# Performance work log

Measured on AMD Instinct MI355X. Metric: run time of the kernel, lower is better.

The kernel has to match this reference:

```python
import jax, jax.numpy as jnp
import numpy as np

N_DT, N_OD = 30000, 10000
D_DT, D_OD = 128, 64
H, O = 128, 64
E1, E2, EL = 500000, 300000, 200000


def _w(k, shape):
    return jax.random.normal(k, shape, jnp.float32) / np.sqrt(shape[0]).astype(np.float32)


def setup_inputs() -> dict:
    key = jax.random.key(0)
    ks = jax.random.split(key, 32)
    inp = {
        "x_dt": jax.random.normal(ks[0], (N_DT, D_DT), jnp.float32),
        "x_od": jax.random.normal(ks[1], (N_OD, D_OD), jnp.float32),
        "ei_dt": jax.random.randint(ks[2], (2, E1), 0, N_DT),
        "ei_rev_src": jax.random.randint(ks[3], (E2,), 0, N_DT),
        "ei_rev_dst": jax.random.randint(ks[4], (E2,), 0, N_OD),
        "el_src": jax.random.randint(ks[5], (EL,), 0, N_OD),
        "el_dst": jax.random.randint(ks[6], (EL,), 0, N_DT),
        # ODEncoderModel params
        "od1_wl": _w(ks[7], (D_DT, H)), "od1_wr": _w(ks[8], (D_DT, H)), "od1_b": jnp.zeros((H,), jnp.float32),
        "od2_wl": _w(ks[9], (H, H)),    "od2_wr": _w(ks[10], (D_OD, H)), "od2_b": jnp.zeros((H,), jnp.float32),
        "od3_wl": _w(ks[11], (H, H)),   "od3_wr": _w(ks[12], (H, H)),    "od3_b": jnp.zeros((H,), jnp.float32),
        "od_lw": _w(ks[13], (H, O)),    "od_lb": jnp.zeros((O,), jnp.float32),
        # DetectorTimeEncoder params
        "dt1_wl": _w(ks[14], (D_DT, H)), "dt1_wr": _w(ks[15], (D_DT, H)), "dt1_b": jnp.zeros((H,), jnp.float32),
        "dt2_wl": _w(ks[16], (H, H)),    "dt2_wr": _w(ks[17], (H, H)),    "dt2_b": jnp.zeros((H,), jnp.float32),
        "dt_lw": _w(ks[18], (H, O)),     "dt_lb": jnp.zeros((O,), jnp.float32),
        # EdgeDecoder params (hidden = out_channels = O)
        "dec_w1": _w(ks[19], (2 * O, O)), "dec_b1": jnp.zeros((O,), jnp.float32),
        "dec_w2": _w(ks[20], (O, 1)),     "dec_b2": jnp.zeros((1,), jnp.float32),
    }
    return inp


def sage(x_src, x_dst, row, col, wl, wr, b, n_dst):
    """PyG SAGEConv (aggr='mean', root_weight=True): lin_l(mean_j x_src[j]) + lin_r(x_dst)."""
    msg = jax.ops.segment_sum(x_src[row], col, num_segments=n_dst)  # [n_dst, d_src]
    cnt = jax.ops.segment_sum(jnp.ones_like(col, dtype=x_src.dtype), col, num_segments=n_dst)
    agg = msg / jnp.maximum(cnt, 1.0)[:, None]
    return agg @ wl + x_dst @ wr + b


def reference(x_dt, x_od, ei_dt, ei_rev_src, ei_rev_dst, el_src, el_dst,
              od1_wl, od1_wr, od1_b, od2_wl, od2_wr, od2_b, od3_wl, od3_wr, od3_b, od_lw, od_lb,
              dt1_wl, dt1_wr, dt1_b, dt2_wl, dt2_wr, dt2_b, dt_lw, dt_lb,
              dec_w1, dec_b1, dec_w2, dec_b2):
    r1, c1 = ei_dt[0], ei_dt[1]
    relu = jax.nn.relu
    # OD encoder: dt metapath conv, then two bipartite convs dt->od
    h = relu(sage(x_dt, x_dt, r1, c1, od1_wl, od1_wr, od1_b, N_DT))
    od = relu(sage(h, x_od, ei_rev_src, ei_rev_dst, od2_wl, od2_wr, od2_b, N_OD))
    od = relu(sage(h, od, ei_rev_src, ei_rev_dst, od3_wl, od3_wr, od3_b, N_OD))
    z_od = od @ od_lw + od_lb  # [N_OD, O]
    # DetectorTime encoder: two homogeneous convs on dt graph
    d = relu(sage(x_dt, x_dt, r1, c1, dt1_wl, dt1_wr, dt1_b, N_DT))
    d = relu(sage(d, d, r1, c1, dt2_wl, dt2_wr, dt2_b, N_DT))
    z_dt = d @ dt_lw + dt_lb  # [N_DT, O]
    # Edge decoder: gather pairs, MLP, sigmoid
    z = jnp.concatenate([z_od[el_src], z_dt[el_dst]], axis=-1)  # [EL, 2O]
    z = relu(z @ dec_w1 + dec_b1)
    return jax.nn.sigmoid(z @ dec_w2 + dec_b2).reshape(-1)  # [EL]
```

## Files before the change

### kernel.cpp

```cpp
#include <hip/hip_runtime.h>
#include <hip/hip_bf16.h>

#define NDT 30000
#define NOD 10000
#define NE1 500000
#define NE2 300000
#define NEL 200000
#define CAP_DT 64
#define CAP_OD 96

typedef unsigned short ushort_t;
typedef unsigned int uint_t;
typedef __attribute__((ext_vector_type(8))) short short8;
typedef __attribute__((ext_vector_type(4))) float f32x4;

static constexpr size_t F_BFUSE = 0;
static constexpr size_t F_ENDF  = 64;
static constexpr size_t U_XDT    = 0;
static constexpr size_t U_XOD    = U_XDT + (size_t)NDT * 128;
static constexpr size_t U_AGGX   = U_XOD + (size_t)NOD * 64;
static constexpr size_t U_H      = U_AGGX + (size_t)NDT * 128;
static constexpr size_t U_D1     = U_H + (size_t)NDT * 128;
static constexpr size_t U_AGGH   = U_D1 + (size_t)NDT * 128;
static constexpr size_t U_OD2    = U_AGGH + (size_t)NOD * 128;
static constexpr size_t U_OD3    = U_OD2 + (size_t)NOD * 128;
static constexpr size_t U_WT1A   = U_OD3 + (size_t)NOD * 128;
static constexpr size_t U_WT1B   = U_WT1A + 32768;
static constexpr size_t U_WTOD2  = U_WT1B + 32768;
static constexpr size_t U_WTOD3  = U_WTOD2 + 24576;
static constexpr size_t U_WTDT2  = U_WTOD3 + 32768;
static constexpr size_t U_WLODT  = U_WTDT2 + 32768;
static constexpr size_t U_WLDTT  = U_WLODT + 8192;
static constexpr size_t U_POD    = U_WLDTT + 8192;
static constexpr size_t U_PDT    = U_POD + (size_t)NOD * 64;
static constexpr size_t U_SRC_DT = U_PDT + (size_t)NDT * 64;
static constexpr size_t U_SRC_OD = U_SRC_DT + (size_t)NDT * CAP_DT;
static constexpr size_t U_END    = U_SRC_OD + (size_t)NOD * CAP_OD;
static constexpr size_t I_CNT_DT = 0;
static constexpr size_t I_CNT_OD = 30000;

__device__ __forceinline__ ushort_t f2bf(float f) {
    uint_t u = __float_as_uint(f);
    return (ushort_t)((u + 0x7fffu + ((u >> 16) & 1u)) >> 16);
}
__device__ __forceinline__ float bf2f(uint_t lo16) { return __uint_as_float(lo16 << 16); }

static constexpr int NB_FILL = (NE1 / 4 + 255) / 256;
static constexpr int NB_CONV = ((NDT * 128 + NOD * 64) / 4 + 255) / 256;
static constexpr int NB_WT   = (155648 + 255) / 256;
static constexpr int NB_FUSE = (16448 + 255) / 256;
static constexpr int NB_PF   = NB_FILL + NB_CONV + NB_WT + NB_FUSE;

struct PFArgs {
    const int *r1, *c1, *rev_src, *rev_dst;
    int *cnt_dt, *cnt_od;
    ushort_t *srcs_dt, *srcs_od;
    const float *x_dt, *x_od;
    ushort_t *xdt_bf, *xod_bf;
    const float *od1_wl, *od1_wr, *dt1_wl, *dt1_wr;
    const float *od2_wl, *od2_wr, *od3_wl, *od3_wr, *dt2_wl, *dt2_wr;
    ushort_t *wt1a, *wt1b, *wtod2, *wtod3, *wtdt2;
    const float *od_lw, *od_lb, *dt_lw, *dt_lb, *w1, *b1;
    ushort_t *wodt, *wdtt;
    float *bfuse;
};

__global__ __launch_bounds__(256) void prep_fill(PFArgs p) {
    int blk = blockIdx.x;
    int tid = threadIdx.x;
    if (blk < NB_FILL) {
        int b = (blk * 256 + tid) * 4;
        if (b + 3 < NE1) {
            int4 d = *(const int4*)(p.c1 + b);
            int4 s = *(const int4*)(p.r1 + b);
            int p0 = atomicAdd(&p.cnt_dt[d.x], 1);
            int p1 = atomicAdd(&p.cnt_dt[d.y], 1);
            int p2 = atomicAdd(&p.cnt_dt[d.z], 1);
            int p3 = atomicAdd(&p.cnt_dt[d.w], 1);
            if (p0 < CAP_DT) p.srcs_dt[d.x * CAP_DT + p0] = (ushort_t)s.x;
            if (p1 < CAP_DT) p.srcs_dt[d.y * CAP_DT + p1] = (ushort_t)s.y;
            if (p2 < CAP_DT) p.srcs_dt[d.z * CAP_DT + p2] = (ushort_t)s.z;
            if (p3 < CAP_DT) p.srcs_dt[d.w * CAP_DT + p3] = (ushort_t)s.w;
        } else {
            for (int i = b; i < NE1; i++) {
                int q = atomicAdd(&p.cnt_dt[p.c1[i]], 1);
                if (q < CAP_DT) p.srcs_dt[p.c1[i] * CAP_DT + q] = (ushort_t)p.r1[i];
            }
        }
        if (b + 3 < NE2) {
            int4 d = *(const int4*)(p.rev_dst + b);
            int4 s = *(const int4*)(p.rev_src + b);
            int p0 = atomicAdd(&p.cnt_od[d.x], 1);
            int p1 = atomicAdd(&p.cnt_od[d.y], 1);
            int p2 = atomicAdd(&p.cnt_od[d.z], 1);
            int p3 = atomicAdd(&p.cnt_od[d.w], 1);
            if (p0 < CAP_OD) p.srcs_od[d.x * CAP_OD + p0] = (ushort_t)s.x;
            if (p1 < CAP_OD) p.srcs_od[d.y * CAP_OD + p1] = (ushort_t)s.y;
            if (p2 < CAP_OD) p.srcs_od[d.z * CAP_OD + p2] = (ushort_t)s.z;
            if (p3 < CAP_OD) p.srcs_od[d.w * CAP_OD + p3] = (ushort_t)s.w;
        } else if (b < NE2) {
            for (int i = b; i < NE2; i++) {
                int q = atomicAdd(&p.cnt_od[p.rev_dst[i]], 1);
                if (q < CAP_OD) p.srcs_od[p.rev_dst[i] * CAP_OD + q] = (ushort_t)p.rev_src[i];
            }
        }
        return;
    }
    blk -= NB_FILL;
    if (blk < NB_CONV) {
        size_t i4 = ((size_t)blk * 256 + tid) * 4;
        const size_t n_dt = (size_t)NDT * 128, n_od = (size_t)NOD * 64;
        if (i4 < n_dt) {
            float4 v = *(const float4*)(p.x_dt + i4);
            ushort4 o = { f2bf(v.x), f2bf(v.y), f2bf(v.z), f2bf(v.w) };
            *(ushort4*)(p.xdt_bf + i4) = o;
        } else if (i4 - n_dt < n_od) {
            size_t j = i4 - n_dt;
            float4 v = *(const float4*)(p.x_od + j);
            ushort4 o = { f2bf(v.x), f2bf(v.y), f2bf(v.z), f2bf(v.w) };
            *(ushort4*)(p.xod_bf + j) = o;
        }
        return;
    }
    blk -= NB_CONV;
    if (blk < NB_WT) {
        int i = blk * 256 + tid;
        const float* wl; const float* wr; ushort_t* dst; int q, KT;
        if (i < 32768)       { q = i;          KT = 256; wl = p.od1_wl; wr = p.od1_wr; dst = p.wt1a; }
        else if (i < 65536)  { q = i - 32768;  KT = 256; wl = p.dt1_wl; wr = p.dt1_wr; dst = p.wt1b; }
        else if (i < 90112)  { q = i - 65536;  KT = 192; wl = p.od2_wl; wr = p.od2_wr; dst = p.wtod2; }
        else if (i < 122880) { q = i - 90112;  KT = 256; wl = p.od3_wl; wr = p.od3_wr; dst = p.wtod3; }
        else if (i < 155648) { q = i - 122880; KT = 256; wl = p.dt2_wl; wr = p.dt2_wr; dst = p.wtdt2; }
        else return;
        int n = q / KT, k = q - n * KT;
        float v = (k < 128) ? wl[(size_t)k * 128 + n] : wr[(size_t)(k - 128) * 128 + n];
        dst[q] = f2bf(v);
        return;
    }
    blk -= NB_WT;
    {
        int i = blk * 256 + tid;
        if (i < 8192) {
            int r = i >> 6, q = i & 63;
            float s = 0.f;
            for (int j = 0; j < 64; j++) s = fmaf(p.od_lw[r * 64 + j], p.w1[j * 64 + q], s);
            p.wodt[q * 128 + r] = f2bf(s);
        } else if (i < 16384) {
            int w = i - 8192, r = w >> 6, q = w & 63;
            float s = 0.f;
            for (int j = 0; j < 64; j++) s = fmaf(p.dt_lw[r * 64 + j], p.w1[(64 + j) * 64 + q], s);
            p.wdtt[q * 128 + r] = f2bf(s);
        } else if (i < 16448) {
            int q = i - 16384;
            float s = p.b1[q];
            for (int j = 0; j < 64; j++) {
                s = fmaf(p.od_lb[j], p.w1[j * 64 + q], s);
                s = fmaf(p.dt_lb[j], p.w1[(64 + j) * 64 + q], s);
            }
            p.bfuse[q] = s;
        }
    }
}

__device__ __forceinline__ void seg_mean_body(const ushort_t* __restrict__ X,
                                              const int* __restrict__ cnt,
                                              const ushort_t* __restrict__ srcs, int cap,
                                              ushort_t* __restrict__ out, int b, int t) {
    int deg = cnt[b];
    int n = deg < cap ? deg : cap;
    int start = b * cap;
    float lo[8] = {}, hi[8] = {};
    int j = 0;
    for (; j + 7 < n; j += 8) {
        uint_t v[8];
#pragma unroll
        for (int u = 0; u < 8; u++) {
            int s = srcs[start + j + u];
            v[u] = *(const uint_t*)&X[(size_t)s * 128 + 2 * t];
        }
#pragma unroll
        for (int u = 0; u < 8; u++) {
            lo[u] += bf2f(v[u] & 0xffff);
            hi[u] += __uint_as_float(v[u] & 0xffff0000u);
        }
    }
    for (; j < n; j++) {
        uint_t v = *(const uint_t*)&X[(size_t)srcs[start + j] * 128 + 2 * t];
        lo[0] += bf2f(v & 0xffff);
        hi[0] += __uint_as_float(v & 0xffff0000u);
    }
    float inv = deg > 0 ? 1.f / (float)deg : 0.f;
    float s0 = (((lo[0] + lo[1]) + (lo[2] + lo[3])) + ((lo[4] + lo[5]) + (lo[6] + lo[7]))) * inv;
    float s1 = (((hi[0] + hi[1]) + (hi[2] + hi[3])) + ((hi[4] + hi[5]) + (hi[6] + hi[7]))) * inv;
    *(uint_t*)&out[(size_t)b * 128 + 2 * t] = (uint_t)f2bf(s0) | ((uint_t)f2bf(s1) << 16);
}

__global__ __launch_bounds__(64) void seg_mean_bf(const ushort_t* __restrict__ X,
                                                  const int* __restrict__ cnt,
                                                  const ushort_t* __restrict__ srcs, int cap,
                                                  ushort_t* __restrict__ out) {
    seg_mean_body(X, cnt, srcs, cap, out, blockIdx.x, threadIdx.x);
}

__global__ __launch_bounds__(64) void seg_mean2(const ushort_t* Xa, const int* cnta, const ushort_t* srca,
                                                int capa, ushort_t* outa, int Na,
                                                const ushort_t* Xb, const int* cntb, const ushort_t* srcb,
                                                int capb, ushort_t* outb) {
    int b = blockIdx.x;
    if (b < Na) seg_mean_body(Xa, cnta, srca, capa, outa, b, threadIdx.x);
    else        seg_mean_body(Xb, cntb, srcb, capb, outb, b - Na, threadIdx.x);
}

template <bool DUAL>
__global__ __launch_bounds__(256) void sage_mfma(
    const ushort_t* __restrict__ A1, int K1,
    const ushort_t* __restrict__ A2, int K2,
    const ushort_t* __restrict__ Wta, const ushort_t* __restrict__ Wtb,
    const float* __restrict__ ba, const float* __restrict__ bb,
    ushort_t* __restrict__ outa, ushort_t* __restrict__ outb, int M) {
    __shared__ __align__(16) ushort_t As[32 * 264];
    __shared__ __align__(16) ushort_t Wsa[128 * 40];
    __shared__ __align__(16) ushort_t Wsb[DUAL ? 128 * 40 : 8];
    const int KT = K1 + K2;
    const int AST = KT + 8;
    int t = threadIdx.x;
    int lane = t & 63, wave = t >> 6;
    int quad = lane >> 4, l16 = lane & 15;
    int mtile = wave & 1, nquad = wave >> 1;
    int mb = blockIdx.x * 32;

    int c1n = 32 * (K1 >> 3);
    for (int c = t; c < c1n; c += 256) {
        int row = c / (K1 >> 3), k8 = (c % (K1 >> 3)) * 8;
        int m = mb + row; if (m >= M) m = M - 1;
        *(short8*)&As[row * AST + k8] = *(const short8*)&A1[(size_t)m * K1 + k8];
    }
    int c2n = 32 * (K2 >> 3);
    for (int c = t; c < c2n; c += 256) {
        int row = c / (K2 >> 3), k8 = (c % (K2 >> 3)) * 8;
        int m = mb + row; if (m >= M) m = M - 1;
        *(short8*)&As[row * AST + K1 + k8] = *(const short8*)&A2[(size_t)m * K2 + k8];
    }
    f32x4 acca[4] = {};
    f32x4 accb[4] = {};
    for (int kc = 0; kc < KT; kc += 32) {
        __syncthreads();
        for (int c = t; c < 512; c += 256) {
            int n = c >> 2, k8 = (c & 3) * 8;
            *(short8*)&Wsa[n * 40 + k8] = *(const short8*)&Wta[(size_t)n * KT + kc + k8];
            if (DUAL)
                *(short8*)&Wsb[n * 40 + k8] = *(const short8*)&Wtb[(size_t)n * KT + kc + k8];
        }
        __syncthreads();
        short8 af = *(const short8*)&As[(mtile * 16 + l16) * AST + kc + quad * 8];
#pragma unroll
        for (int nt = 0; nt < 4; nt++) {
            int n = (nquad * 4 + nt) * 16 + l16;
            short8 bfr = *(const short8*)&Wsa[n * 40 + quad * 8];
            acca[nt] = __builtin_amdgcn_mfma_f32_16x16x32_bf16(af, bfr, acca[nt], 0, 0, 0);
            if (DUAL) {
                short8 bfr2 = *(const short8*)&Wsb[n * 40 + quad * 8];
                accb[nt] = __builtin_amdgcn_mfma_f32_16x16x32_bf16(af, bfr2, accb[nt], 0, 0, 0);
            }
        }
    }
    int mrow = mb + mtile * 16 + quad * 4;
#pragma unroll
    for (int nt = 0; nt < 4; nt++) {
        int n = (nquad * 4 + nt) * 16 + l16;
        float bva = ba[n];
        float bvb = DUAL ? bb[n] : 0.f;
#pragma unroll
        for (int r = 0; r < 4; r++) {
            int m = mrow + r;
            if (m < M) {
                outa[(size_t)m * 128 + n] = f2bf(fmaxf(acca[nt][r] + bva, 0.f));
                if (DUAL) outb[(size_t)m * 128 + n] = f2bf(fmaxf(accb[nt][r] + bvb, 0.f));
            }
        }
    }
}

struct SageJob {
    const ushort_t *A1, *A2;
    int K1, K2;
    const ushort_t *Wt;
    const float *bias;
    ushort_t *out;
    int M;
};

__global__ __launch_bounds__(256) void sage_two(SageJob ja, int nb_a, SageJob jb) {
    __shared__ __align__(16) ushort_t As[32 * 264];
    __shared__ __align__(16) ushort_t Wsa[128 * 40];
    SageJob j;
    int blk;
    if (blockIdx.x < nb_a) { j = ja; blk = blockIdx.x; }
    else                   { j = jb; blk = blockIdx.x - nb_a; }
    const int KT = j.K1 + j.K2;
    const int AST = KT + 8;
    int t = threadIdx.x;
    int lane = t & 63, wave = t >> 6;
    int quad = lane >> 4, l16 = lane & 15;
    int mtile = wave & 1, nquad = wave >> 1;
    int mb = blk * 32;

    int c1n = 32 * (j.K1 >> 3);
    for (int c = t; c < c1n; c += 256) {
        int row = c / (j.K1 >> 3), k8 = (c % (j.K1 >> 3)) * 8;
        int m = mb + row; if (m >= j.M) m = j.M - 1;
        *(short8*)&As[row * AST + k8] = *(const short8*)&j.A1[(size_t)m * j.K1 + k8];
    }
    int c2n = 32 * (j.K2 >> 3);
    for (int c = t; c < c2n; c += 256) {
        int row = c / (j.K2 >> 3), k8 = (c % (j.K2 >> 3)) * 8;
        int m = mb + row; if (m >= j.M) m = j.M - 1;
        *(short8*)&As[row * AST + j.K1 + k8] = *(const short8*)&j.A2[(size_t)m * j.K2 + k8];
    }
    f32x4 acc[4] = {};
    for (int kc = 0; kc < KT; kc += 32) {
        __syncthreads();
        for (int c = t; c < 512; c += 256) {
            int n = c >> 2, k8 = (c & 3) * 8;
            *(short8*)&Wsa[n * 40 + k8] = *(const short8*)&j.Wt[(size_t)n * KT + kc + k8];
        }
        __syncthreads();
        short8 af = *(const short8*)&As[(mtile * 16 + l16) * AST + kc + quad * 8];
#pragma unroll
        for (int nt = 0; nt < 4; nt++) {
            int n = (nquad * 4 + nt) * 16 + l16;
            short8 bfr = *(const short8*)&Wsa[n * 40 + quad * 8];
            acc[nt] = __builtin_amdgcn_mfma_f32_16x16x32_bf16(af, bfr, acc[nt], 0, 0, 0);
        }
    }
    int mrow = mb + mtile * 16 + quad * 4;
#pragma unroll
    for (int nt = 0; nt < 4; nt++) {
        int n = (nquad * 4 + nt) * 16 + l16;
        float bv = j.bias[n];
#pragma unroll
        for (int r = 0; r < 4; r++) {
            int m = mrow + r;
            if (m < j.M) j.out[(size_t)m * 128 + n] = f2bf(fmaxf(acc[nt][r] + bv, 0.f));
        }
    }
}

struct LinJob {
    const ushort_t *A, *Wt;
    ushort_t *out;
    int M;
};

__device__ __forceinline__ void lin_body(const LinJob& j, int blk, int t) {
    __shared__ __align__(16) ushort_t As[64 * 136];
    __shared__ __align__(16) ushort_t Ws[64 * 40];
    int lane = t & 63, wave = t >> 6;
    int quad = lane >> 4, l16 = lane & 15;
    int mb = blk * 64;
    for (int c = t; c < 1024; c += 256) {
        int row = c >> 4, k8 = (c & 15) * 8;
        int m = mb + row; if (m >= j.M) m = j.M - 1;
        *(short8*)&As[row * 136 + k8] = *(const short8*)&j.A[(size_t)m * 128 + k8];
    }
    f32x4 acc[4] = {};
    for (int kc = 0; kc < 128; kc += 32) {
        __syncthreads();
        for (int c = t; c < 256; c += 256) {
            int n = c >> 2, k8 = (c & 3) * 8;
            *(short8*)&Ws[n * 40 + k8] = *(const short8*)&j.Wt[(size_t)n * 128 + kc + k8];
        }
        __syncthreads();
        short8 af = *(const short8*)&As[(wave * 16 + l16) * 136 + kc + quad * 8];
#pragma unroll
        for (int nt = 0; nt < 4; nt++) {
            short8 bfr = *(const short8*)&Ws[(nt * 16 + l16) * 40 + quad * 8];
            acc[nt] = __builtin_amdgcn_mfma_f32_16x16x32_bf16(af, bfr, acc[nt], 0, 0, 0);
        }
    }
    int mrow = mb + wave * 16 + quad * 4;
#pragma unroll
    for (int nt = 0; nt < 4; nt++) {
        int n = nt * 16 + l16;
#pragma unroll
        for (int r = 0; r < 4; r++) {
            int m = mrow + r;
            if (m < j.M) j.out[(size_t)m * 64 + n] = f2bf(acc[nt][r]);
        }
    }
}

__global__ __launch_bounds__(256) void lin_two(LinJob ja, int nb_a, LinJob jb) {
    if (blockIdx.x < nb_a) lin_body(ja, blockIdx.x, threadIdx.x);
    else                   lin_body(jb, blockIdx.x - nb_a, threadIdx.x);
}

__global__ __launch_bounds__(256) void decode(const ushort_t* __restrict__ P_od, const ushort_t* __restrict__ P_dt,
                                              const int* __restrict__ el_src, const int* __restrict__ el_dst,
                                              const float* __restrict__ bfuse, const float* __restrict__ w2,
                                              const float* __restrict__ b2v, float* __restrict__ out) {
    __shared__ __align__(16) float bf[64];
    __shared__ __align__(16) float w2s[64];
    int t = threadIdx.x;
    if (t < 64) { bf[t] = bfuse[t]; w2s[t] = w2[t]; }
    __syncthreads();
    int e = blockIdx.x * 256 + t;
    if (e >= NEL) return;
    const uint4* po = (const uint4*)(P_od + (size_t)el_src[e] * 64);
    const uint4* pt = (const uint4*)(P_dt + (size_t)el_dst[e] * 64);
    float acc = 0.f;
#pragma unroll
    for (int c = 0; c < 8; c++) {
        uint4 a = po[c], b = pt[c];
        const uint_t* au = (const uint_t*)&a;
        const uint_t* bu = (const uint_t*)&b;
#pragma unroll
        for (int j = 0; j < 4; j++) {
            int idx = c * 8 + j * 2;
            float lo = bf2f(au[j] & 0xffff) + bf2f(bu[j] & 0xffff) + bf[idx];
            float hi = __uint_as_float(au[j] & 0xffff0000u) + __uint_as_float(bu[j] & 0xffff0000u) + bf[idx + 1];
            acc = fmaf(fmaxf(lo, 0.f), w2s[idx], acc);
            acc = fmaf(fmaxf(hi, 0.f), w2s[idx + 1], acc);
        }
    }
    float z = acc + b2v[0];
    out[e] = 1.f / (1.f + __expf(-z));
}

extern "C" void kernel_launch(void* const* d_in, const int* in_sizes, int n_in,
                              void* d_out, int out_size, void* d_ws, size_t ws_size,
                              hipStream_t stream) {
    float* W = (float*)d_ws;
    ushort_t* U = (ushort_t*)(W + F_ENDF);
    int* I = (int*)(U + U_END);

    const float* x_dt   = (const float*)d_in[0];
    const float* x_od   = (const float*)d_in[1];
    const int* ei       = (const int*)d_in[2];
    const int* r1 = ei;
    const int* c1 = ei + NE1;
    const int* rev_src  = (const int*)d_in[3];
    const int* rev_dst  = (const int*)d_in[4];
    const int* el_src   = (const int*)d_in[5];
    const int* el_dst   = (const int*)d_in[6];
    const float* od1_wl = (const float*)d_in[7],  *od1_wr = (const float*)d_in[8],  *od1_b = (const float*)d_in[9];
    const float* od2_wl = (const float*)d_in[10], *od2_wr = (const float*)d_in[11], *od2_b = (const float*)d_in[12];
    const float* od3_wl = (const float*)d_in[13], *od3_wr = (const float*)d_in[14], *od3_b = (const float*)d_in[15];
    const float* od_lw  = (const float*)d_in[16], *od_lb  = (const float*)d_in[17];
    const float* dt1_wl = (const float*)d_in[18], *dt1_wr = (const float*)d_in[19], *dt1_b = (const float*)d_in[20];
    const float* dt2_wl = (const float*)d_in[21], *dt2_wr = (const float*)d_in[22], *dt2_b = (const float*)d_in[23];
    const float* dt_lw  = (const float*)d_in[24], *dt_lb  = (const float*)d_in[25];
    const float* dec_w1 = (const float*)d_in[26], *dec_b1 = (const float*)d_in[27];
    const float* dec_w2 = (const float*)d_in[28], *dec_b2 = (const float*)d_in[29];

    hipMemsetAsync(I + I_CNT_DT, 0, (NDT + NOD) * sizeof(int), stream);

    PFArgs p;
    p.r1 = r1; p.c1 = c1; p.rev_src = rev_src; p.rev_dst = rev_dst;
    p.cnt_dt = I + I_CNT_DT; p.cnt_od = I + I_CNT_OD;
    p.srcs_dt = U + U_SRC_DT; p.srcs_od = U + U_SRC_OD;
    p.x_dt = x_dt; p.x_od = x_od;
    p.xdt_bf = U + U_XDT; p.xod_bf = U + U_XOD;
    p.od1_wl = od1_wl; p.od1_wr = od1_wr; p.dt1_wl = dt1_wl; p.dt1_wr = dt1_wr;
    p.od2_wl = od2_wl; p.od2_wr = od2_wr; p.od3_wl = od3_wl; p.od3_wr = od3_wr;
    p.dt2_wl = dt2_wl; p.dt2_wr = dt2_wr;
    p.wt1a = U + U_WT1A; p.wt1b = U + U_WT1B; p.wtod2 = U + U_WTOD2;
    p.wtod3 = U + U_WTOD3; p.wtdt2 = U + U_WTDT2;
    p.od_lw = od_lw; p.od_lb = od_lb; p.dt_lw = dt_lw; p.dt_lb = dt_lb;
    p.w1 = dec_w1; p.b1 = dec_b1;
    p.wodt = U + U_WLODT; p.wdtt = U + U_WLDTT;
    p.bfuse = W + F_BFUSE;
    prep_fill<<<NB_PF, 256, 0, stream>>>(p);

    seg_mean_bf<<<NDT, 64, 0, stream>>>(U + U_XDT, I + I_CNT_DT, U + U_SRC_DT, CAP_DT, U + U_AGGX);
    sage_mfma<true><<<(NDT + 31) / 32, 256, 0, stream>>>(U + U_AGGX, 128, U + U_XDT, 128,
                                                         U + U_WT1A, U + U_WT1B, od1_b, dt1_b,
                                                         U + U_H, U + U_D1, NDT);
    seg_mean2<<<NDT + NOD, 64, 0, stream>>>(U + U_D1, I + I_CNT_DT, U + U_SRC_DT, CAP_DT, U + U_AGGX, NDT,
                                            U + U_H, I + I_CNT_OD, U + U_SRC_OD, CAP_OD, U + U_AGGH);
    {
        SageJob jd2 = { U + U_AGGX, U + U_D1, 128, 128, U + U_WTDT2, dt2_b, U + U_H, NDT };
        SageJob jod2 = { U + U_AGGH, U + U_XOD, 128, 64, U + U_WTOD2, od2_b, U + U_OD2, NOD };
        int nb_d2 = (NDT + 31) / 32;
        int nb_od2 = (NOD + 31) / 32;
        sage_two<<<nb_d2 + nb_od2, 256, 0, stream>>>(jd2, nb_d2, jod2);
    }
    sage_mfma<false><<<(NOD + 31) / 32, 256, 0, stream>>>(U + U_AGGH, 128, U + U_OD2, 128,
                                                          U + U_WTOD3, nullptr, od3_b, nullptr,
                                                          U + U_OD3, nullptr, NOD);
    {
        LinJob jdt = { U + U_H, U + U_WLDTT, U + U_PDT, NDT };
        LinJob jod = { U + U_OD3, U + U_WLODT, U + U_POD, NOD };
        int nb_dt = (NDT + 63) / 64;
        int nb_od = (NOD + 63) / 64;
        lin_two<<<nb_dt + nb_od, 256, 0, stream>>>(jdt, nb_dt, jod);
    }
    decode<<<(NEL + 255) / 256, 256, 0, stream>>>(U + U_POD, U + U_PDT, el_src, el_dst,
                                                  W + F_BFUSE, dec_w2, dec_b2, (float*)d_out);
}
```

Baseline: 279.5 us.

## Fuse final 128->64 linear projections into epilogue of last SAGE layers

Removes the separate lin_two kernel by letting sage_two write its ReLU'd bf16 tile into shared memory and immediately multiply by the 64-column output weight, emitting the projected rows directly. The dt2 layer no longer writes its hidden activations to global memory, and the od3 layer runs through sage_two with the fused projection instead of sage_mfma. This saves one launch and a global write/read of the 30000x128 and 10000x128 hidden tensors, at the cost of extra shared memory, an extra sync and more work in the epilogue.

```diff
diff --git a/kernel.cpp b/kernel.cpp
--- a/kernel.cpp
+++ b/kernel.cpp
@@ -23,8 +23,7 @@
 static constexpr size_t U_D1     = U_H + (size_t)NDT * 128;
 static constexpr size_t U_AGGH   = U_D1 + (size_t)NDT * 128;
 static constexpr size_t U_OD2    = U_AGGH + (size_t)NOD * 128;
-static constexpr size_t U_OD3    = U_OD2 + (size_t)NOD * 128;
-static constexpr size_t U_WT1A   = U_OD3 + (size_t)NOD * 128;
+static constexpr size_t U_WT1A   = U_OD2 + (size_t)NOD * 128;
 static constexpr size_t U_WT1B   = U_WT1A + 32768;
 static constexpr size_t U_WTOD2  = U_WT1B + 32768;
 static constexpr size_t U_WTOD3  = U_WTOD2 + 24576;
@@ -288,11 +287,13 @@
     const float *bias;
     ushort_t *out;
     int M;
+    const ushort_t *Wlin;
+    ushort_t *Pout;
 };
 
 __global__ __launch_bounds__(256) void sage_two(SageJob ja, int nb_a, SageJob jb) {
     __shared__ __align__(16) ushort_t As[32 * 264];
-    __shared__ __align__(16) ushort_t Wsa[128 * 40];
+    __shared__ __align__(16) ushort_t Wsa[64 * 136];
     SageJob j;
     int blk;
     if (blockIdx.x < nb_a) { j = ja; blk = blockIdx.x; }
@@ -334,65 +335,58 @@
         }
     }
     int mrow = mb + mtile * 16 + quad * 4;
+    if (!j.Wlin) {
+#pragma unroll
+        for (int nt = 0; nt < 4; nt++) {
+            int n = (nquad * 4 + nt) * 16 + l16;
+            float bv = j.bias[n];
+#pragma unroll
+            for (int r = 0; r < 4; r++) {
+                int m = mrow + r;
+                if (m < j.M) j.out[(size_t)m * 128 + n] = f2bf(fmaxf(acc[nt][r] + bv, 0.f));
+            }
+        }
+        return;
+    }
+    __syncthreads();
 #pragma unroll
     for (int nt = 0; nt < 4; nt++) {
         int n = (nquad * 4 + nt) * 16 + l16;
         float bv = j.bias[n];
 #pragma unroll
         for (int r = 0; r < 4; r++) {
-            int m = mrow + r;
-            if (m < j.M) j.out[(size_t)m * 128 + n] = f2bf(fmaxf(acc[nt][r] + bv, 0.f));
-        }
-    }
-}
-
-struct LinJob {
-    const ushort_t *A, *Wt;
-    ushort_t *out;
-    int M;
-};
-
-__device__ __forceinline__ void lin_body(const LinJob& j, int blk, int t) {
-    __shared__ __align__(16) ushort_t As[64 * 136];
-    __shared__ __align__(16) ushort_t Ws[64 * 40];
-    int lane = t & 63, wave = t >> 6;
-    int quad = lane >> 4, l16 = lane & 15;
-    int mb = blk * 64;
+            int row = mtile * 16 + quad * 4 + r;
+            ushort_t v = f2bf(fmaxf(acc[nt][r] + bv, 0.f));
+            As[row * 136 + n] = v;
+            int m = mb + row;
+            if (j.out && m < j.M) j.out[(size_t)m * 128 + n] = v;
+        }
+    }
     for (int c = t; c < 1024; c += 256) {
         int row = c >> 4, k8 = (c & 15) * 8;
-        int m = mb + row; if (m >= j.M) m = j.M - 1;
-        *(short8*)&As[row * 136 + k8] = *(const short8*)&j.A[(size_t)m * 128 + k8];
-    }
-    f32x4 acc[4] = {};
+        *(short8*)&Wsa[row * 136 + k8] = *(const short8*)&j.Wlin[(size_t)row * 128 + k8];
+    }
+    __syncthreads();
+    f32x4 acc2[2] = {};
+#pragma unroll
     for (int kc = 0; kc < 128; kc += 32) {
-        __syncthreads();
-        for (int c = t; c < 256; c += 256) {
-            int n = c >> 2, k8 = (c & 3) * 8;
-            *(short8*)&Ws[n * 40 + k8] = *(const short8*)&j.Wt[(size_t)n * 128 + kc + k8];
-        }
-        __syncthreads();
-        short8 af = *(const short8*)&As[(wave * 16 + l16) * 136 + kc + quad * 8];
-#pragma unroll
-        for (int nt = 0; nt < 4; nt++) {
-            short8 bfr = *(const short8*)&Ws[(nt * 16 + l16) * 40 + quad * 8];
-            acc[nt] = __builtin_amdgcn_mfma_f32_16x16x32_bf16(af, bfr, acc[nt], 0, 0, 0);
-        }
-    }
-    int mrow = mb + wave * 16 + quad * 4;
-#pragma unroll
-    for (int nt = 0; nt < 4; nt++) {
-        int n = nt * 16 + l16;
+        short8 af = *(const short8*)&As[(mtile * 16 + l16) * 136 + kc + quad * 8];
+#pragma unroll
+        for (int nt = 0; nt < 2; nt++) {
+            int n16 = (wave >> 1) * 2 + nt;
+            short8 bfr = *(const short8*)&Wsa[(n16 * 16 + l16) * 136 + kc + quad * 8];
+            acc2[nt] = __builtin_amdgcn_mfma_f32_16x16x32_bf16(af, bfr, acc2[nt], 0, 0, 0);
+        }
+    }
+#pragma unroll
+    for (int nt = 0; nt < 2; nt++) {
+        int n = ((wave >> 1) * 2 + nt) * 16 + l16;
 #pragma unroll
         for (int r = 0; r < 4; r++) {
             int m = mrow + r;
-            if (m < j.M) j.out[(size_t)m * 64 + n] = f2bf(acc[nt][r]);
-        }
-    }
-}
-
-__global__ __launch_bounds__(256) void lin_two(LinJob ja, int nb_a, LinJob jb) {
-    if (blockIdx.x < nb_a) lin_body(ja, blockIdx.x, threadIdx.x);
-    else                   lin_body(jb, blockIdx.x - nb_a, threadIdx.x);
+            if (m < j.M) j.Pout[(size_t)m * 64 + n] = f2bf(acc2[nt][r]);
+        }
+    }
 }
 
 __global__ __launch_bounds__(256) void decode(const ushort_t* __restrict__ P_od, const ushort_t* __restrict__ P_dt,
@@ -479,21 +473,19 @@
     seg_mean2<<<NDT + NOD, 64, 0, stream>>>(U + U_D1, I + I_CNT_DT, U + U_SRC_DT, CAP_DT, U + U_AGGX, NDT,
                                             U + U_H, I + I_CNT_OD, U + U_SRC_OD, CAP_OD, U + U_AGGH);
     {
-        SageJob jd2 = { U + U_AGGX, U + U_D1, 128, 128, U + U_WTDT2, dt2_b, U + U_H, NDT };
-        SageJob jod2 = { U + U_AGGH, U + U_XOD, 128, 64, U + U_WTOD2, od2_b, U + U_OD2, NOD };
+        SageJob jd2 = { U + U_AGGX, U + U_D1, 128, 128, U + U_WTDT2, dt2_b, nullptr, NDT,
+                        U + U_WLDTT, U + U_PDT };
+        SageJob jod2 = { U + U_AGGH, U + U_XOD, 128, 64, U + U_WTOD2, od2_b, U + U_OD2, NOD,
+                         nullptr, nullptr };
         int nb_d2 = (NDT + 31) / 32;
         int nb_od2 = (NOD + 31) / 32;
         sage_two<<<nb_d2 + nb_od2, 256, 0, stream>>>(jd2, nb_d2, jod2);
     }
-    sage_mfma<false><<<(NOD + 31) / 32, 256, 0, stream>>>(U + U_AGGH, 128, U + U_OD2, 128,
-                                                          U + U_WTOD3, nullptr, od3_b, nullptr,
-                                                          U + U_OD3, nullptr, NOD);
     {
-        LinJob jdt = { U + U_H, U + U_WLDTT, U + U_PDT, NDT };
-        LinJob jod = { U + U_OD3, U + U_WLODT, U + U_POD, NOD };
-        int nb_dt = (NDT + 63) / 64;
-        int nb_od = (NOD + 63) / 64;
-        lin_two<<<nb_dt + nb_od, 256, 0, stream>>>(jdt, nb_dt, jod);
+        SageJob jod3 = { U + U_AGGH, U + U_OD2, 128, 128, U + U_WTOD3, od3_b, nullptr, NOD,
+                         U + U_WLODT, U + U_POD };
+        int nb = (NOD + 31) / 32;
+        sage_two<<<nb, 256, 0, stream>>>(jod3, nb, jod3);
     }
     decode<<<(NEL + 255) / 256, 256, 0, stream>>>(U + U_POD, U + U_PDT, el_src, el_dst,
                                                   W + F_BFUSE, dec_w2, dec_b2, (float*)d_out);
```

New measurement: 280.8 us. Within noise of the previous version (+0.5%).
